# Optimization experiments

Hardware: AMD Instinct MI355X
Metric: run time of the kernel (lower is better)

The kernel has to match this reference:

```python
import jax, jax.numpy as jnp
import numpy as np

NUM_LEVELS = 16
LEVEL_DIM = 2
BASE_RES = 16
DESIRED_RES = 2048
HASHMAP_SIZE = 2 ** 19
MULTIRES = 6
N_POINTS = 1048576

_scale = np.exp2(np.log2(DESIRED_RES / BASE_RES) / (NUM_LEVELS - 1))
RESOLUTIONS = [int(np.ceil(BASE_RES * _scale ** l)) for l in range(NUM_LEVELS)]
PRIMES = np.array([1, 2654435761, 805459861], dtype=np.uint32)
CORNERS = np.array([[i, j, k] for i in (0, 1) for j in (0, 1) for k in (0, 1)], dtype=np.int32)  # [8,3]


def positional_embed(x):
    # NeRF embedding (include_input, log-sampled freqs 2^0..2^(M-1)) -> [N, 3 + 3*2*M] = [N,39]
    freqs = (2.0 ** jnp.arange(MULTIRES)).astype(x.dtype)        # [M]
    xb = x[:, None, :] * freqs[None, :, None]                    # [N, M, 3]
    emb = jnp.concatenate([jnp.sin(xb), jnp.cos(xb)], axis=-1)   # [N, M, 6]
    return jnp.concatenate([x, emb.reshape(x.shape[0], -1)], axis=-1)


def hash_encode(x, tables):
    # multiresolution hash-grid trilinear lookup; x in [0,1]^3 -> [N, NUM_LEVELS*LEVEL_DIM]
    corners = jnp.asarray(CORNERS)       # [8,3]
    primes = jnp.asarray(PRIMES)         # [3] uint32
    outs = []
    for l, R in enumerate(RESOLUTIONS):  # fixed 16 levels (structurally distinct)
        pos = x * (R - 1)                # [N,3]
        p0 = jnp.floor(pos)
        w = pos - p0                     # fractional part, [N,3]
        c = p0.astype(jnp.int32)[:, None, :] + corners[None]   # [N,8,3] corner coords
        c = jnp.clip(c, 0, R - 1)
        if (R ** 3) <= HASHMAP_SIZE:
            idx = c[..., 0] + R * c[..., 1] + R * R * c[..., 2]  # direct (dense) indexing
        else:
            cu = c.astype(jnp.uint32)
            h = (cu[..., 0] * primes[0]) ^ (cu[..., 1] * primes[1]) ^ (cu[..., 2] * primes[2])
            idx = (h & jnp.uint32(HASHMAP_SIZE - 1)).astype(jnp.int32)
        wc = jnp.where(corners[None].astype(bool), w[:, None, :], 1.0 - w[:, None, :])  # [N,8,3]
        wc = jnp.prod(wc, axis=-1)        # trilinear weights [N,8]
        feats = tables[l][idx]            # gather [N,8,LEVEL_DIM]
        outs.append(jnp.sum(wc[..., None] * feats, axis=1))
    return jnp.concatenate(outs, axis=-1)


def softplus100(x):
    # torch.nn.Softplus(beta=100) with default threshold=20 (linear when beta*x > 20)
    return jnp.where(x * 100.0 > 20.0, x, jax.nn.softplus(x * 100.0) / 100.0)


def setup_inputs() -> dict:
    key = jax.random.key(0)
    ks = jax.random.split(key, 8)
    D_IN = 3 + 3 * 2 * MULTIRES + NUM_LEVELS * LEVEL_DIM  # 71
    x = jax.random.uniform(ks[0], (N_POINTS, 3), dtype=jnp.float32)
    tables = jax.random.uniform(ks[1], (NUM_LEVELS, HASHMAP_SIZE, LEVEL_DIM), minval=-1e-4, maxval=1e-4, dtype=jnp.float32)
    W0 = jax.random.normal(ks[2], (64, D_IN), dtype=jnp.float32) * (np.sqrt(2.0) / np.sqrt(64.0))
    b0 = jnp.zeros((64,), jnp.float32)
    W1 = jax.random.normal(ks[3], (64, 64), dtype=jnp.float32) * (np.sqrt(2.0) / np.sqrt(64.0))
    b1 = jnp.zeros((64,), jnp.float32)
    W2 = jnp.full((17, 64), np.sqrt(np.pi) / np.sqrt(64.0), jnp.float32) + jax.random.normal(ks[4], (17, 64), dtype=jnp.float32) * 1e-4
    b2 = jnp.full((17,), -1.0, jnp.float32)  # geometric init bias
    return {"x": x, "tables": tables, "W0": W0, "b0": b0, "W1": W1, "b1": b1, "W2": W2, "b2": b2}


def reference(x, tables, W0, b0, W1, b1, W2, b2):
    # divide_factor = 1.0 -> encoding sees x directly
    feat = hash_encode(x, tables)                                   # [N,32]
    h = jnp.concatenate([positional_embed(x), feat], axis=-1)       # [N,71]
    h = softplus100(h @ W0.T + b0)                                  # [N,64]
    h = softplus100(h @ W1.T + b1)                                  # [N,64]
    return h @ W2.T + b2                                            # [N,17] = (sdf, 16 features)
```

## Files before the change

### kernel.cpp

```cpp
#include <hip/hip_runtime.h>
#include <stdint.h>

#define HMAP   (1u << 19)
#define HMASK  (HMAP - 1u)

typedef short bf16x8 __attribute__((ext_vector_type(8)));
typedef float f32x4  __attribute__((ext_vector_type(4)));
typedef float f32x2  __attribute__((ext_vector_type(2)));
typedef unsigned u32x2 __attribute__((ext_vector_type(2)));

__device__ __constant__ const int c_res[16] = {16, 23, 31, 43, 59, 81, 112, 154, 213, 295, 407, 562, 777, 1073, 1483, 2048};

__device__ __forceinline__ unsigned short f2bf(float f) {
    unsigned u = __float_as_uint(f);
    u += 0x7fffu + ((u >> 16) & 1u);
    return (unsigned short)(u >> 16);
}

__device__ __forceinline__ float softplus100(float v) {
    return fmaxf(v, 0.f) + 0.01f * __logf(1.f + __expf(-100.f * fabsf(v)));
}

__device__ __forceinline__ bf16x8 cvt8(const float* __restrict__ p) {
    f32x4 a = *(const f32x4*)p;
    f32x4 b = *(const f32x4*)(p + 4);
    bf16x8 r;
    r[0] = f2bf(a[0]); r[1] = f2bf(a[1]); r[2] = f2bf(a[2]); r[3] = f2bf(a[3]);
    r[4] = f2bf(b[0]); r[5] = f2bf(b[1]); r[6] = f2bf(b[2]); r[7] = f2bf(b[3]);
    return r;
}

__device__ __forceinline__ float2 upk(unsigned v) {
    return make_float2(__uint_as_float(v << 16), __uint_as_float(v & 0xffff0000u));
}

__device__ __forceinline__ float2 gather_level(const float* __restrict__ tab, int R,
                                               float x0, float x1, float x2) {
    const float Rm1 = (float)(R - 1);
    float px = x0 * Rm1, py = x1 * Rm1, pz = x2 * Rm1;
    float fx = floorf(px), fy = floorf(py), fz = floorf(pz);
    float wx = px - fx, wy = py - fy, wz = pz - fz;
    int ix = (int)fx, iy = (int)fy, iz = (int)fz;
    ix = max(0, min(ix, R - 1)); iy = max(0, min(iy, R - 1)); iz = max(0, min(iz, R - 1));
    int jx = min(ix + 1, R - 1), jy = min(iy + 1, R - 1), jz = min(iz + 1, R - 1);
    float ax = 1.f - wx, ay = 1.f - wy, az = 1.f - wz;
    float wyz0 = ay * az, wyz1 = wy * az, wyz2 = ay * wz, wyz3 = wy * wz;
    float2 lo[4], hi[4];
    const bool adj = (jx == ix + 1);
    if ((long long)R * R * R <= (long long)HMAP) {
        unsigned sy = (unsigned)R, sz = (unsigned)(R * R);
        unsigned bases[4] = {(unsigned)iy * sy + (unsigned)iz * sz,
                             (unsigned)jy * sy + (unsigned)iz * sz,
                             (unsigned)iy * sy + (unsigned)jz * sz,
                             (unsigned)jy * sy + (unsigned)jz * sz};
        const float2* t2 = (const float2*)tab;
        #pragma unroll
        for (int k = 0; k < 4; ++k) {
            unsigned i0 = bases[k] + (unsigned)ix;
            if (adj && !(i0 & 1u)) {
                f32x4 q = *(const f32x4*)(tab + ((size_t)i0 << 1));
                lo[k] = make_float2(q[0], q[1]);
                hi[k] = make_float2(q[2], q[3]);
            } else {
                lo[k] = t2[i0];
                hi[k] = t2[bases[k] + (unsigned)jx];
            }
        }
    } else {
        unsigned hy0 = (unsigned)iy * 2654435761u, hy1 = (unsigned)jy * 2654435761u;
        unsigned hz0 = (unsigned)iz * 805459861u,  hz1 = (unsigned)jz * 805459861u;
        unsigned ms[4] = {hy0 ^ hz0, hy1 ^ hz0, hy0 ^ hz1, hy1 ^ hz1};
        if (adj && ((ix & 1) == 0)) {
            #pragma unroll
            for (int k = 0; k < 4; ++k) {
                unsigned h = ((unsigned)ix ^ ms[k]) & HMASK;
                f32x4 q = *(const f32x4*)(tab + ((size_t)(h & ~1u) << 1));
                float2 e0 = make_float2(q[0], q[1]);
                float2 e1 = make_float2(q[2], q[3]);
                bool sw = (h & 1u) != 0;
                lo[k] = sw ? e1 : e0;
                hi[k] = sw ? e0 : e1;
            }
        } else {
            const float2* t2 = (const float2*)tab;
            #pragma unroll
            for (int k = 0; k < 4; ++k) {
                unsigned hl = ((unsigned)ix ^ ms[k]) & HMASK;
                unsigned hh = ((unsigned)jx ^ ms[k]) & HMASK;
                lo[k] = t2[hl];
                hi[k] = t2[hh];
            }
        }
    }
    float2 r = make_float2(0.f, 0.f);
    float wyz[4] = {wyz0, wyz1, wyz2, wyz3};
    #pragma unroll
    for (int k = 0; k < 4; ++k) {
        float wl = ax * wyz[k], wh = wx * wyz[k];
        r.x += wl * lo[k].x + wh * hi[k].x;
        r.y += wl * lo[k].y + wh * hi[k].y;
    }
    return r;
}

__device__ __forceinline__ void gather2(const float* __restrict__ tab, int R,
                                        float x0A, float x1A, float x2A,
                                        float x0B, float x1B, float x2B,
                                        float2& rA, float2& rB) {
    const float Rm1 = (float)(R - 1);
    float wxv[2], axv[2];
    float wyz[2][4];
    float2 lo[2][4], hi[2][4];
    int ixv[2], jxv[2];
    unsigned basev[2][4];
    const bool dense = (long long)R * R * R <= (long long)HMAP;
    #pragma unroll
    for (int t = 0; t < 2; ++t) {
        const float X0 = t ? x0B : x0A, X1 = t ? x1B : x1A, X2 = t ? x2B : x2A;
        float px = X0 * Rm1, py = X1 * Rm1, pz = X2 * Rm1;
        float fx = floorf(px), fy = floorf(py), fz = floorf(pz);
        float wx = px - fx, wy = py - fy, wz = pz - fz;
        int ix = (int)fx, iy = (int)fy, iz = (int)fz;
        ix = max(0, min(ix, R - 1)); iy = max(0, min(iy, R - 1)); iz = max(0, min(iz, R - 1));
        int jx = min(ix + 1, R - 1), jy = min(iy + 1, R - 1), jz = min(iz + 1, R - 1);
        float ax = 1.f - wx, ay = 1.f - wy, az = 1.f - wz;
        wyz[t][0] = ay * az; wyz[t][1] = wy * az; wyz[t][2] = ay * wz; wyz[t][3] = wy * wz;
        wxv[t] = wx; axv[t] = ax; ixv[t] = ix; jxv[t] = jx;
        if (dense) {
            unsigned sy = (unsigned)R, sz = (unsigned)(R * R);
            basev[t][0] = (unsigned)iy * sy + (unsigned)iz * sz;
            basev[t][1] = (unsigned)jy * sy + (unsigned)iz * sz;
            basev[t][2] = (unsigned)iy * sy + (unsigned)jz * sz;
            basev[t][3] = (unsigned)jy * sy + (unsigned)jz * sz;
        } else {
            unsigned hy0 = (unsigned)iy * 2654435761u, hy1 = (unsigned)jy * 2654435761u;
            unsigned hz0 = (unsigned)iz * 805459861u,  hz1 = (unsigned)jz * 805459861u;
            basev[t][0] = hy0 ^ hz0; basev[t][1] = hy1 ^ hz0;
            basev[t][2] = hy0 ^ hz1; basev[t][3] = hy1 ^ hz1;
        }
    }
    if (dense) {
        const float2* t2 = (const float2*)tab;
        #pragma unroll
        for (int t = 0; t < 2; ++t) {
            const bool adj = (jxv[t] == ixv[t] + 1);
            #pragma unroll
            for (int k = 0; k < 4; ++k) {
                unsigned i0 = basev[t][k] + (unsigned)ixv[t];
                if (adj && !(i0 & 1u)) {
                    f32x4 q = *(const f32x4*)(tab + ((size_t)i0 << 1));
                    lo[t][k] = make_float2(q[0], q[1]);
                    hi[t][k] = make_float2(q[2], q[3]);
                } else {
                    lo[t][k] = t2[i0];
                    hi[t][k] = t2[basev[t][k] + (unsigned)jxv[t]];
                }
            }
        }
    } else {
        const float2* t2 = (const float2*)tab;
        #pragma unroll
        for (int t = 0; t < 2; ++t) {
            const bool adj = (jxv[t] == ixv[t] + 1) && ((ixv[t] & 1) == 0);
            #pragma unroll
            for (int k = 0; k < 4; ++k) {
                if (adj) {
                    unsigned h = ((unsigned)ixv[t] ^ basev[t][k]) & HMASK;
                    f32x4 q = *(const f32x4*)(tab + ((size_t)(h & ~1u) << 1));
                    float2 e0 = make_float2(q[0], q[1]);
                    float2 e1 = make_float2(q[2], q[3]);
                    bool sw = (h & 1u) != 0;
                    lo[t][k] = sw ? e1 : e0;
                    hi[t][k] = sw ? e0 : e1;
                } else {
                    unsigned hl = ((unsigned)ixv[t] ^ basev[t][k]) & HMASK;
                    unsigned hh = ((unsigned)jxv[t] ^ basev[t][k]) & HMASK;
                    lo[t][k] = t2[hl];
                    hi[t][k] = t2[hh];
                }
            }
        }
    }
    float2 res[2];
    #pragma unroll
    for (int t = 0; t < 2; ++t) {
        float2 r = make_float2(0.f, 0.f);
        #pragma unroll
        for (int k = 0; k < 4; ++k) {
            float wl = axv[t] * wyz[t][k], wh = wxv[t] * wyz[t][k];
            r.x += wl * lo[t][k].x + wh * hi[t][k].x;
            r.y += wl * lo[t][k].y + wh * hi[t][k].y;
        }
        res[t] = r;
    }
    rA = res[0]; rB = res[1];
}

__device__ __forceinline__ void gather2h(const unsigned* __restrict__ tab, int R,
                                         float x0A, float x1A, float x2A,
                                         float x0B, float x1B, float x2B,
                                         float2& rA, float2& rB) {
    const float Rm1 = (float)(R - 1);
    float wxv[2], axv[2], wyz[2][4];
    int ixv[2], jxv[2];
    bool adjv[2];
    unsigned msv[2][4];
    #pragma unroll
    for (int t = 0; t < 2; ++t) {
        const float X0 = t ? x0B : x0A, X1 = t ? x1B : x1A, X2 = t ? x2B : x2A;
        float px = X0 * Rm1, py = X1 * Rm1, pz = X2 * Rm1;
        float fx = floorf(px), fy = floorf(py), fz = floorf(pz);
        float wx = px - fx, wy = py - fy, wz = pz - fz;
        int ix = (int)fx, iy = (int)fy, iz = (int)fz;
        ix = max(0, min(ix, R - 1)); iy = max(0, min(iy, R - 1)); iz = max(0, min(iz, R - 1));
        int jx = min(ix + 1, R - 1), jy = min(iy + 1, R - 1), jz = min(iz + 1, R - 1);
        float ax = 1.f - wx, ay = 1.f - wy, az = 1.f - wz;
        wyz[t][0] = ay * az; wyz[t][1] = wy * az; wyz[t][2] = ay * wz; wyz[t][3] = wy * wz;
        wxv[t] = wx; axv[t] = ax; ixv[t] = ix; jxv[t] = jx;
        adjv[t] = (jx == ix + 1) && ((ix & 1) == 0);
        unsigned hy0 = (unsigned)iy * 2654435761u, hy1 = (unsigned)jy * 2654435761u;
        unsigned hz0 = (unsigned)iz * 805459861u,  hz1 = (unsigned)jz * 805459861u;
        msv[t][0] = hy0 ^ hz0; msv[t][1] = hy1 ^ hz0;
        msv[t][2] = hy0 ^ hz1; msv[t][3] = hy1 ^ hz1;
    }
    float2 lo[2][4], hi[2][4];
    #pragma unroll
    for (int t = 0; t < 2; ++t) {
        #pragma unroll
        for (int k = 0; k < 4; ++k) {
            if (adjv[t]) {
                unsigned h = ((unsigned)ixv[t] ^ msv[t][k]) & HMASK;
                u32x2 q = *(const u32x2*)(tab + (h & ~1u));
                float2 e0 = upk(q[0]), e1 = upk(q[1]);
                bool sw = (h & 1u) != 0;
                lo[t][k] = sw ? e1 : e0;
                hi[t][k] = sw ? e0 : e1;
            } else {
                unsigned hl = ((unsigned)ixv[t] ^ msv[t][k]) & HMASK;
                unsigned hh = ((unsigned)jxv[t] ^ msv[t][k]) & HMASK;
                lo[t][k] = upk(tab[hl]);
                hi[t][k] = upk(tab[hh]);
            }
        }
    }
    float2 res[2];
    #pragma unroll
    for (int t = 0; t < 2; ++t) {
        float2 r = make_float2(0.f, 0.f);
        #pragma unroll
        for (int k = 0; k < 4; ++k) {
            float wl = axv[t] * wyz[t][k], wh = wxv[t] * wyz[t][k];
            r.x += wl * lo[t][k].x + wh * hi[t][k].x;
            r.y += wl * lo[t][k].y + wh * hi[t][k].y;
        }
        res[t] = r;
    }
    rA = res[0]; rB = res[1];
}

__global__ __launch_bounds__(256)
void cvt_tables(const float* __restrict__ tables, unsigned* __restrict__ tbf) {
    const size_t i = (size_t)blockIdx.x * 256 + threadIdx.x;
    const f32x2* src = (const f32x2*)(tables + (size_t)5 * 2 * HMAP);
    f32x2 f = __builtin_nontemporal_load(src + i);
    unsigned v = (unsigned)f2bf(f[0]) | ((unsigned)f2bf(f[1]) << 16);
    __builtin_nontemporal_store(v, tbf + i);
}

__global__ __launch_bounds__(256, 6)
void gather_hashed(const float* __restrict__ x, const unsigned* __restrict__ tbf,
                   unsigned* __restrict__ feat, int N) {
    const int j = blockIdx.x & 7;
    const int i = blockIdx.x >> 3;
    int level, chunk;
    if (i < 2048) {
        level = 5 + j; chunk = i;
    } else {
        const int r = i - 2048;
        if (j < 3) {
            const int share = (j == 2) ? 682 : 683;
            if (r >= share) return;
            level = 13; chunk = j * 683 + r;
        } else if (j < 6) {
            const int jj = j - 3;
            const int share = (jj == 2) ? 682 : 683;
            if (r >= share) return;
            level = 14; chunk = jj * 683 + r;
        } else {
            if (r >= 1024) return;
            level = 15; chunk = (j - 6) * 1024 + r;
        }
    }
    const size_t p0 = (size_t)chunk * 512 + 2u * threadIdx.x;
    const f32x2* xv = (const f32x2*)(x + 3 * p0);
    f32x2 u0 = __builtin_nontemporal_load(xv);
    f32x2 u1 = __builtin_nontemporal_load(xv + 1);
    f32x2 u2 = __builtin_nontemporal_load(xv + 2);
    float2 fA, fB;
    gather2h(tbf + (size_t)(level - 5) * HMAP, c_res[level],
             u0[0], u0[1], u1[0],
             u1[1], u2[0], u2[1],
             fA, fB);
    u32x2 v;
    v[0] = (unsigned)f2bf(fA.x) | ((unsigned)f2bf(fA.y) << 16);
    v[1] = (unsigned)f2bf(fB.x) | ((unsigned)f2bf(fB.y) << 16);
    __builtin_nontemporal_store(v, (u32x2*)(feat + (size_t)(level - 5) * N + p0));
}

#define NPB       128
#define TILES     8
#define PTS_BLK   (NPB * TILES)
#define SA_STRIDE 104
#define SW0_OFF   (128 * 104)
#define SMEM_SHORTS (SW0_OFF + 64 * 104)

__global__ __launch_bounds__(256, 4)
void mlp_tiled2(const float* __restrict__ x, const float* __restrict__ tables,
                const unsigned* __restrict__ feat,
                const float* __restrict__ W0, const float* __restrict__ b0,
                const float* __restrict__ W1, const float* __restrict__ b1,
                const float* __restrict__ W2, const float* __restrict__ b2,
                float* __restrict__ out, int N) {
    __shared__ unsigned short smem[SMEM_SHORTS];
    const int tid  = threadIdx.x;
    const int blk  = blockIdx.x;
    const int wave = tid >> 6, lane = tid & 63;
    const int mhalf = (wave & 1) * 64;
    const int nhalf = (wave >> 1);
    const int lrow = lane & 15, quad = lane >> 4;

    for (int i = tid; i < 64 * 104; i += 256) {
        int n = i / 104, k = i - n * 104;
        smem[SW0_OFF + i] = (k < 71) ? f2bf(W0[n * 71 + k]) : (unsigned short)0;
    }
    for (int i = tid; i < 128 * 25; i += 256) {
        int p = i / 25, k = i - p * 25;
        smem[p * SA_STRIDE + 71 + k] = 0;
    }
    bf16x8 w1f[2][2];
    #pragma unroll
    for (int ks = 0; ks < 2; ++ks)
        #pragma unroll
        for (int nt = 0; nt < 2; ++nt) {
            int n = nhalf * 32 + nt * 16 + lrow;
            w1f[ks][nt] = cvt8(W1 + n * 64 + ks * 32 + quad * 8);
        }
    bf16x8 w2f[2];
    {
        int n2 = nhalf * 16 + lrow;
        #pragma unroll
        for (int ks = 0; ks < 2; ++ks) {
            if (n2 < 17) w2f[ks] = cvt8(W2 + n2 * 64 + ks * 32 + quad * 8);
            else { bf16x8 z = {0,0,0,0,0,0,0,0}; w2f[ks] = z; }
        }
    }
    float b0v[2], b1v[2], b2v;
    #pragma unroll
    for (int nt = 0; nt < 2; ++nt) {
        b0v[nt] = b0[nhalf * 32 + nt * 16 + lrow];
        b1v[nt] = b1[nhalf * 32 + nt * 16 + lrow];
    }
    { int c2 = nhalf * 16 + lrow; b2v = (c2 < 17) ? b2[c2] : 0.f; }
    __syncthreads();

    const size_t pbase0 = (size_t)blk * PTS_BLK;
    #pragma unroll 1
    for (int t = 0; t < TILES; ++t) {
        const size_t pb = pbase0 + (size_t)t * NPB;
        {
            const int p = tid & 127;
            const size_t gp = pb + p;
            unsigned short* row = &smem[p * SA_STRIDE];
            const float x0 = __builtin_nontemporal_load(x + 3 * gp);
            const float x1 = __builtin_nontemporal_load(x + 3 * gp + 1);
            const float x2 = __builtin_nontemporal_load(x + 3 * gp + 2);
            float sa, ca, sb, cb, sc, cc;
            __sincosf(x0, &sa, &ca);
            __sincosf(x1, &sb, &cb);
            __sincosf(x2, &sc, &cc);
            if (tid < 128) {
                row[0] = f2bf(x0); row[1] = f2bf(x1); row[2] = f2bf(x2);
                #pragma unroll
                for (int m = 0; m < 6; ++m) {
                    row[3 + 6 * m + 0] = f2bf(sa);
                    row[3 + 6 * m + 1] = f2bf(sb);
                    row[3 + 6 * m + 2] = f2bf(sc);
                    float nsa = 2.f * sa * ca, nca = 1.f - 2.f * sa * sa;
                    float nsb = 2.f * sb * cb, ncb = 1.f - 2.f * sb * sb;
                    float nsc = 2.f * sc * cc, ncc = 1.f - 2.f * sc * sc;
                    sa = nsa; ca = nca; sb = nsb; cb = ncb; sc = nsc; cc = ncc;
                }
                float2 f;
                f = gather_level(tables,                         16, x0, x1, x2);
                row[39] = f2bf(f.x); row[40] = f2bf(f.y);
                f = gather_level(tables + (size_t)1 * 2 * HMAP,  23, x0, x1, x2);
                row[41] = f2bf(f.x); row[42] = f2bf(f.y);
                f = gather_level(tables + (size_t)2 * 2 * HMAP,  31, x0, x1, x2);
                row[43] = f2bf(f.x); row[44] = f2bf(f.y);
            } else {
                #pragma unroll
                for (int m = 0; m < 6; ++m) {
                    row[3 + 6 * m + 3] = f2bf(ca);
                    row[3 + 6 * m + 4] = f2bf(cb);
                    row[3 + 6 * m + 5] = f2bf(cc);
                    float nsa = 2.f * sa * ca, nca = 1.f - 2.f * sa * sa;
                    float nsb = 2.f * sb * cb, ncb = 1.f - 2.f * sb * sb;
                    float nsc = 2.f * sc * cc, ncc = 1.f - 2.f * sc * sc;
                    sa = nsa; ca = nca; sb = nsb; cb = ncb; sc = nsc; cc = ncc;
                }
                float2 f;
                f = gather_level(tables + (size_t)3 * 2 * HMAP,  43, x0, x1, x2);
                row[45] = f2bf(f.x); row[46] = f2bf(f.y);
                f = gather_level(tables + (size_t)4 * 2 * HMAP,  59, x0, x1, x2);
                row[47] = f2bf(f.x); row[48] = f2bf(f.y);
                #pragma unroll
                for (int li = 0; li < 11; ++li) {
                    unsigned v = __builtin_nontemporal_load(feat + (size_t)li * N + gp);
                    row[49 + 2 * li] = (unsigned short)(v & 0xffffu);
                    row[50 + 2 * li] = (unsigned short)(v >> 16);
                }
            }
        }
        __syncthreads();

        f32x4 acc0[4][2];
        #pragma unroll
        for (int mt = 0; mt < 4; ++mt)
            #pragma unroll
            for (int nt = 0; nt < 2; ++nt) acc0[mt][nt] = (f32x4){0.f, 0.f, 0.f, 0.f};
        #pragma unroll
        for (int ks = 0; ks < 3; ++ks) {
            bf16x8 bfr[2];
            #pragma unroll
            for (int nt = 0; nt < 2; ++nt) {
                int n = nhalf * 32 + nt * 16 + lrow;
                bfr[nt] = *(const bf16x8*)&smem[SW0_OFF + n * 104 + ks * 32 + quad * 8];
            }
            #pragma unroll
            for (int mt = 0; mt < 4; ++mt) {
                int m = mhalf + mt * 16 + lrow;
                bf16x8 afr = *(const bf16x8*)&smem[m * SA_STRIDE + ks * 32 + quad * 8];
                #pragma unroll
                for (int nt = 0; nt < 2; ++nt)
                    acc0[mt][nt] = __builtin_amdgcn_mfma_f32_16x16x32_bf16(afr, bfr[nt], acc0[mt][nt], 0, 0, 0);
            }
        }
        __syncthreads();
        #pragma unroll
        for (int mt = 0; mt < 4; ++mt)
            #pragma unroll
            for (int nt = 0; nt < 2; ++nt) {
                int colg = nhalf * 32 + nt * 16 + lrow;
                #pragma unroll
                for (int r = 0; r < 4; ++r) {
                    int rowm = mhalf + mt * 16 + quad * 4 + r;
                    smem[rowm * SA_STRIDE + colg] = f2bf(softplus100(acc0[mt][nt][r] + b0v[nt]));
                }
            }
        __syncthreads();

        f32x4 acc1[4][2];
        #pragma unroll
        for (int mt = 0; mt < 4; ++mt)
            #pragma unroll
            for (int nt = 0; nt < 2; ++nt) acc1[mt][nt] = (f32x4){0.f, 0.f, 0.f, 0.f};
        #pragma unroll
        for (int ks = 0; ks < 2; ++ks) {
            #pragma unroll
            for (int mt = 0; mt < 4; ++mt) {
                int m = mhalf + mt * 16 + lrow;
                bf16x8 afr = *(const bf16x8*)&smem[m * SA_STRIDE + ks * 32 + quad * 8];
                #pragma unroll
                for (int nt = 0; nt < 2; ++nt)
                    acc1[mt][nt] = __builtin_amdgcn_mfma_f32_16x16x32_bf16(afr, w1f[ks][nt], acc1[mt][nt], 0, 0, 0);
            }
        }
        __syncthreads();
        #pragma unroll
        for (int mt = 0; mt < 4; ++mt)
            #pragma unroll
            for (int nt = 0; nt < 2; ++nt) {
                int colg = nhalf * 32 + nt * 16 + lrow;
                #pragma unroll
                for (int r = 0; r < 4; ++r) {
                    int rowm = mhalf + mt * 16 + quad * 4 + r;
                    smem[rowm * SA_STRIDE + colg] = f2bf(softplus100(acc1[mt][nt][r] + b1v[nt]));
                }
            }
        __syncthreads();

        f32x4 acc2[4];
        #pragma unroll
        for (int mt = 0; mt < 4; ++mt) acc2[mt] = (f32x4){0.f, 0.f, 0.f, 0.f};
        #pragma unroll
        for (int ks = 0; ks < 2; ++ks) {
            #pragma unroll
            for (int mt = 0; mt < 4; ++mt) {
                int m = mhalf + mt * 16 + lrow;
                bf16x8 afr = *(const bf16x8*)&smem[m * SA_STRIDE + ks * 32 + quad * 8];
                acc2[mt] = __builtin_amdgcn_mfma_f32_16x16x32_bf16(afr, w2f[ks], acc2[mt], 0, 0, 0);
            }
        }
        {
            int colg = nhalf * 16 + lrow;
            if (colg < 17) {
                #pragma unroll
                for (int mt = 0; mt < 4; ++mt)
                    #pragma unroll
                    for (int r = 0; r < 4; ++r) {
                        int rowm = mhalf + mt * 16 + quad * 4 + r;
                        __builtin_nontemporal_store(acc2[mt][r] + b2v,
                                                    out + (pb + rowm) * 17 + colg);
                    }
            }
        }
        __syncthreads();
    }
}

__global__ __launch_bounds__(256, 6)
void gather_levels(const float* __restrict__ x, const float* __restrict__ tables,
                   unsigned* __restrict__ feat, int N, int C) {
    const int b = blockIdx.x;
    const int half = 8 * C;
    int r, level;
    if (b < half) { r = b; level = r & 7; }
    else          { r = b - half; level = 15 - (r & 7); }
    const size_t p0 = (size_t)(r >> 3) * 512 + 2u * threadIdx.x;
    const f32x2* xv = (const f32x2*)(x + 3 * p0);
    f32x2 u0 = __builtin_nontemporal_load(xv);
    f32x2 u1 = __builtin_nontemporal_load(xv + 1);
    f32x2 u2 = __builtin_nontemporal_load(xv + 2);
    float2 fA, fB;
    gather2(tables + (size_t)level * (2u * HMAP), c_res[level],
            u0[0], u0[1], u1[0],
            u1[1], u2[0], u2[1],
            fA, fB);
    u32x2 v;
    v[0] = (unsigned)f2bf(fA.x) | ((unsigned)f2bf(fA.y) << 16);
    v[1] = (unsigned)f2bf(fB.x) | ((unsigned)f2bf(fB.y) << 16);
    __builtin_nontemporal_store(v, (u32x2*)(feat + (size_t)level * N + p0));
}

__global__ __launch_bounds__(256, 4)
void mlp_tiled(const float* __restrict__ x, const unsigned* __restrict__ feat,
               const float* __restrict__ W0, const float* __restrict__ b0,
               const float* __restrict__ W1, const float* __restrict__ b1,
               const float* __restrict__ W2, const float* __restrict__ b2,
               float* __restrict__ out, int N) {
    __shared__ unsigned short smem[SMEM_SHORTS];
    const int tid  = threadIdx.x;
    const int blk  = blockIdx.x;
    const int wave = tid >> 6, lane = tid & 63;
    const int mhalf = (wave & 1) * 64;
    const int nhalf = (wave >> 1);
    const int lrow = lane & 15, quad = lane >> 4;

    for (int i = tid; i < 64 * 104; i += 256) {
        int n = i / 104, k = i - n * 104;
        smem[SW0_OFF + i] = (k < 71) ? f2bf(W0[n * 71 + k]) : (unsigned short)0;
    }
    for (int i = tid; i < 128 * 25; i += 256) {
        int p = i / 25, k = i - p * 25;
        smem[p * SA_STRIDE + 71 + k] = 0;
    }
    bf16x8 w1f[2][2];
    #pragma unroll
    for (int ks = 0; ks < 2; ++ks)
        #pragma unroll
        for (int nt = 0; nt < 2; ++nt) {
            int n = nhalf * 32 + nt * 16 + lrow;
            w1f[ks][nt] = cvt8(W1 + n * 64 + ks * 32 + quad * 8);
        }
    bf16x8 w2f[2];
    {
        int n2 = nhalf * 16 + lrow;
        #pragma unroll
        for (int ks = 0; ks < 2; ++ks) {
            if (n2 < 17) w2f[ks] = cvt8(W2 + n2 * 64 + ks * 32 + quad * 8);
            else { bf16x8 z = {0,0,0,0,0,0,0,0}; w2f[ks] = z; }
        }
    }
    float b0v[2], b1v[2], b2v;
    #pragma unroll
    for (int nt = 0; nt < 2; ++nt) {
        b0v[nt] = b0[nhalf * 32 + nt * 16 + lrow];
        b1v[nt] = b1[nhalf * 32 + nt * 16 + lrow];
    }
    { int c2 = nhalf * 16 + lrow; b2v = (c2 < 17) ? b2[c2] : 0.f; }
    __syncthreads();

    const size_t pbase0 = (size_t)blk * PTS_BLK;
    #pragma unroll 1
    for (int t = 0; t < TILES; ++t) {
        const size_t pb = pbase0 + (size_t)t * NPB;
        {
            const int p = tid & 127;
            const size_t gp = pb + p;
            unsigned short* row = &smem[p * SA_STRIDE];
            const float x0 = __builtin_nontemporal_load(x + 3 * gp);
            const float x1 = __builtin_nontemporal_load(x + 3 * gp + 1);
            const float x2 = __builtin_nontemporal_load(x + 3 * gp + 2);
            if (tid < 128) {
                row[0] = f2bf(x0); row[1] = f2bf(x1); row[2] = f2bf(x2);
                float fr = 1.f;
                #pragma unroll
                for (int m = 0; m < 6; ++m) {
                    row[3 + 6 * m + 0] = f2bf(__sinf(x0 * fr));
                    row[3 + 6 * m + 1] = f2bf(__sinf(x1 * fr));
                    row[3 + 6 * m + 2] = f2bf(__sinf(x2 * fr));
                    fr *= 2.f;
                }
            } else {
                float fr = 1.f;
                #pragma unroll
                for (int m = 0; m < 6; ++m) {
                    row[3 + 6 * m + 3] = f2bf(__cosf(x0 * fr));
                    row[3 + 6 * m + 4] = f2bf(__cosf(x1 * fr));
                    row[3 + 6 * m + 5] = f2bf(__cosf(x2 * fr));
                    fr *= 2.f;
                }
                #pragma unroll
                for (int l = 0; l < 16; ++l) {
                    unsigned v = __builtin_nontemporal_load(feat + (size_t)l * N + gp);
                    row[39 + 2 * l] = (unsigned short)(v & 0xffffu);
                    row[40 + 2 * l] = (unsigned short)(v >> 16);
                }
            }
        }
        __syncthreads();

        f32x4 acc0[4][2];
        #pragma unroll
        for (int mt = 0; mt < 4; ++mt)
            #pragma unroll
            for (int nt = 0; nt < 2; ++nt) acc0[mt][nt] = (f32x4){0.f, 0.f, 0.f, 0.f};
        #pragma unroll
        for (int ks = 0; ks < 3; ++ks) {
            bf16x8 bfr[2];
            #pragma unroll
            for (int nt = 0; nt < 2; ++nt) {
                int n = nhalf * 32 + nt * 16 + lrow;
                bfr[nt] = *(const bf16x8*)&smem[SW0_OFF + n * 104 + ks * 32 + quad * 8];
            }
            #pragma unroll
            for (int mt = 0; mt < 4; ++mt) {
                int m = mhalf + mt * 16 + lrow;
                bf16x8 afr = *(const bf16x8*)&smem[m * SA_STRIDE + ks * 32 + quad * 8];
                #pragma unroll
                for (int nt = 0; nt < 2; ++nt)
                    acc0[mt][nt] = __builtin_amdgcn_mfma_f32_16x16x32_bf16(afr, bfr[nt], acc0[mt][nt], 0, 0, 0);
            }
        }
        __syncthreads();
        #pragma unroll
        for (int mt = 0; mt < 4; ++mt)
            #pragma unroll
            for (int nt = 0; nt < 2; ++nt) {
                int colg = nhalf * 32 + nt * 16 + lrow;
                #pragma unroll
                for (int r = 0; r < 4; ++r) {
                    int rowm = mhalf + mt * 16 + quad * 4 + r;
                    smem[rowm * SA_STRIDE + colg] = f2bf(softplus100(acc0[mt][nt][r] + b0v[nt]));
                }
            }
        __syncthreads();

        f32x4 acc1[4][2];
        #pragma unroll
        for (int mt = 0; mt < 4; ++mt)
            #pragma unroll
            for (int nt = 0; nt < 2; ++nt) acc1[mt][nt] = (f32x4){0.f, 0.f, 0.f, 0.f};
        #pragma unroll
        for (int ks = 0; ks < 2; ++ks) {
            #pragma unroll
            for (int mt = 0; mt < 4; ++mt) {
                int m = mhalf + mt * 16 + lrow;
                bf16x8 afr = *(const bf16x8*)&smem[m * SA_STRIDE + ks * 32 + quad * 8];
                #pragma unroll
                for (int nt = 0; nt < 2; ++nt)
                    acc1[mt][nt] = __builtin_amdgcn_mfma_f32_16x16x32_bf16(afr, w1f[ks][nt], acc1[mt][nt], 0, 0, 0);
            }
        }
        __syncthreads();
        #pragma unroll
        for (int mt = 0; mt < 4; ++mt)
            #pragma unroll
            for (int nt = 0; nt < 2; ++nt) {
                int colg = nhalf * 32 + nt * 16 + lrow;
                #pragma unroll
                for (int r = 0; r < 4; ++r) {
                    int rowm = mhalf + mt * 16 + quad * 4 + r;
                    smem[rowm * SA_STRIDE + colg] = f2bf(softplus100(acc1[mt][nt][r] + b1v[nt]));
                }
            }
        __syncthreads();

        f32x4 acc2[4];
        #pragma unroll
        for (int mt = 0; mt < 4; ++mt) acc2[mt] = (f32x4){0.f, 0.f, 0.f, 0.f};
        #pragma unroll
        for (int ks = 0; ks < 2; ++ks) {
            #pragma unroll
            for (int mt = 0; mt < 4; ++mt) {
                int m = mhalf + mt * 16 + lrow;
                bf16x8 afr = *(const bf16x8*)&smem[m * SA_STRIDE + ks * 32 + quad * 8];
                acc2[mt] = __builtin_amdgcn_mfma_f32_16x16x32_bf16(afr, w2f[ks], acc2[mt], 0, 0, 0);
            }
        }
        {
            int colg = nhalf * 16 + lrow;
            if (colg < 17) {
                #pragma unroll
                for (int mt = 0; mt < 4; ++mt)
                    #pragma unroll
                    for (int r = 0; r < 4; ++r) {
                        int rowm = mhalf + mt * 16 + quad * 4 + r;
                        __builtin_nontemporal_store(acc2[mt][r] + b2v,
                                                    out + (pb + rowm) * 17 + colg);
                    }
            }
        }
        __syncthreads();
    }
}

__global__ __launch_bounds__(256, 3)
void gn_fused(const float* __restrict__ x, const float* __restrict__ tables,
              const float* __restrict__ W0, const float* __restrict__ b0,
              const float* __restrict__ W1, const float* __restrict__ b1,
              const float* __restrict__ W2, const float* __restrict__ b2,
              float* __restrict__ out) {
    __shared__ unsigned short smem[SMEM_SHORTS];
    const int tid = threadIdx.x;
    const int blk = blockIdx.x;
    const int wave = tid >> 6, lane = tid & 63;
    const int mhalf = (wave & 1) * 64;
    const int nhalf = (wave >> 1);
    const int lrow = lane & 15, quad = lane >> 4;
    for (int i = tid; i < 64 * 104; i += 256) {
        int n = i / 104, k = i - n * 104;
        smem[SW0_OFF + i] = (k < 71) ? f2bf(W0[n * 71 + k]) : (unsigned short)0;
    }
    for (int i = tid; i < 128 * 25; i += 256) {
        int p = i / 25, k = i - p * 25;
        smem[p * SA_STRIDE + 71 + k] = 0;
    }
    bf16x8 w1f[2][2];
    #pragma unroll
    for (int ks = 0; ks < 2; ++ks)
        #pragma unroll
        for (int nt = 0; nt < 2; ++nt) {
            int n = nhalf * 32 + nt * 16 + lrow;
            w1f[ks][nt] = cvt8(W1 + n * 64 + ks * 32 + quad * 8);
        }
    bf16x8 w2f[2];
    {
        int n2 = nhalf * 16 + lrow;
        #pragma unroll
        for (int ks = 0; ks < 2; ++ks) {
            if (n2 < 17) w2f[ks] = cvt8(W2 + n2 * 64 + ks * 32 + quad * 8);
            else { bf16x8 z = {0,0,0,0,0,0,0,0}; w2f[ks] = z; }
        }
    }
    float b0v[2], b1v[2], b2v;
    #pragma unroll
    for (int nt = 0; nt < 2; ++nt) {
        b0v[nt] = b0[nhalf * 32 + nt * 16 + lrow];
        b1v[nt] = b1[nhalf * 32 + nt * 16 + lrow];
    }
    { int c2 = nhalf * 16 + lrow; b2v = (c2 < 17) ? b2[c2] : 0.f; }
    {
        const int p = tid & 127;
        const size_t gp = (size_t)blk * NPB + p;
        const float x0 = x[3 * gp], x1 = x[3 * gp + 1], x2 = x[3 * gp + 2];
        unsigned short* row = &smem[p * SA_STRIDE];
        if (tid < 128) {
            row[0] = f2bf(x0); row[1] = f2bf(x1); row[2] = f2bf(x2);
            float fr = 1.f;
            #pragma unroll
            for (int m = 0; m < 6; ++m) {
                row[3 + 6 * m + 0] = f2bf(__sinf(x0 * fr));
                row[3 + 6 * m + 1] = f2bf(__sinf(x1 * fr));
                row[3 + 6 * m + 2] = f2bf(__sinf(x2 * fr));
                fr *= 2.f;
            }
            #pragma unroll
            for (int li = 0; li < 8; ++li) {
                const int l = 2 * li;
                float2 f = gather_level(tables + (size_t)l * (2u * HMAP), c_res[l], x0, x1, x2);
                row[39 + 2 * l] = f2bf(f.x);
                row[40 + 2 * l] = f2bf(f.y);
            }
        } else {
            float fr = 1.f;
            #pragma unroll
            for (int m = 0; m < 6; ++m) {
                row[3 + 6 * m + 3] = f2bf(__cosf(x0 * fr));
                row[3 + 6 * m + 4] = f2bf(__cosf(x1 * fr));
                row[3 + 6 * m + 5] = f2bf(__cosf(x2 * fr));
                fr *= 2.f;
            }
            #pragma unroll
            for (int li = 0; li < 8; ++li) {
                const int l = 2 * li + 1;
                float2 f = gather_level(tables + (size_t)l * (2u * HMAP), c_res[l], x0, x1, x2);
                row[39 + 2 * l] = f2bf(f.x);
                row[40 + 2 * l] = f2bf(f.y);
            }
        }
    }
    __syncthreads();
    f32x4 acc0[4][2];
    #pragma unroll
    for (int mt = 0; mt < 4; ++mt)
        #pragma unroll
        for (int nt = 0; nt < 2; ++nt) acc0[mt][nt] = (f32x4){0.f, 0.f, 0.f, 0.f};
    #pragma unroll
    for (int ks = 0; ks < 3; ++ks) {
        bf16x8 bfr[2];
        #pragma unroll
        for (int nt = 0; nt < 2; ++nt) {
            int n = nhalf * 32 + nt * 16 + lrow;
            bfr[nt] = *(const bf16x8*)&smem[SW0_OFF + n * 104 + ks * 32 + quad * 8];
        }
        #pragma unroll
        for (int mt = 0; mt < 4; ++mt) {
            int m = mhalf + mt * 16 + lrow;
            bf16x8 afr = *(const bf16x8*)&smem[m * SA_STRIDE + ks * 32 + quad * 8];
            #pragma unroll
            for (int nt = 0; nt < 2; ++nt)
                acc0[mt][nt] = __builtin_amdgcn_mfma_f32_16x16x32_bf16(afr, bfr[nt], acc0[mt][nt], 0, 0, 0);
        }
    }
    __syncthreads();
    #pragma unroll
    for (int mt = 0; mt < 4; ++mt)
        #pragma unroll
        for (int nt = 0; nt < 2; ++nt) {
            int colg = nhalf * 32 + nt * 16 + lrow;
            #pragma unroll
            for (int r = 0; r < 4; ++r) {
                int rowm = mhalf + mt * 16 + quad * 4 + r;
                smem[rowm * SA_STRIDE + colg] = f2bf(softplus100(acc0[mt][nt][r] + b0v[nt]));
            }
        }
    __syncthreads();
    f32x4 acc1[4][2];
    #pragma unroll
    for (int mt = 0; mt < 4; ++mt)
        #pragma unroll
        for (int nt = 0; nt < 2; ++nt) acc1[mt][nt] = (f32x4){0.f, 0.f, 0.f, 0.f};
    #pragma unroll
    for (int ks = 0; ks < 2; ++ks) {
        #pragma unroll
        for (int mt = 0; mt < 4; ++mt) {
            int m = mhalf + mt * 16 + lrow;
            bf16x8 afr = *(const bf16x8*)&smem[m * SA_STRIDE + ks * 32 + quad * 8];
            #pragma unroll
            for (int nt = 0; nt < 2; ++nt)
                acc1[mt][nt] = __builtin_amdgcn_mfma_f32_16x16x32_bf16(afr, w1f[ks][nt], acc1[mt][nt], 0, 0, 0);
        }
    }
    __syncthreads();
    #pragma unroll
    for (int mt = 0; mt < 4; ++mt)
        #pragma unroll
        for (int nt = 0; nt < 2; ++nt) {
            int colg = nhalf * 32 + nt * 16 + lrow;
            #pragma unroll
            for (int r = 0; r < 4; ++r) {
                int rowm = mhalf + mt * 16 + quad * 4 + r;
                smem[rowm * SA_STRIDE + colg] = f2bf(softplus100(acc1[mt][nt][r] + b1v[nt]));
            }
        }
    __syncthreads();
    f32x4 acc2[4];
    #pragma unroll
    for (int mt = 0; mt < 4; ++mt) acc2[mt] = (f32x4){0.f, 0.f, 0.f, 0.f};
    #pragma unroll
    for (int ks = 0; ks < 2; ++ks) {
        #pragma unroll
        for (int mt = 0; mt < 4; ++mt) {
            int m = mhalf + mt * 16 + lrow;
            bf16x8 afr = *(const bf16x8*)&smem[m * SA_STRIDE + ks * 32 + quad * 8];
            acc2[mt] = __builtin_amdgcn_mfma_f32_16x16x32_bf16(afr, w2f[ks], acc2[mt], 0, 0, 0);
        }
    }
    {
        int colg = nhalf * 16 + lrow;
        if (colg < 17) {
            #pragma unroll
            for (int mt = 0; mt < 4; ++mt)
                #pragma unroll
                for (int r = 0; r < 4; ++r) {
                    int rowm = mhalf + mt * 16 + quad * 4 + r;
                    out[((size_t)blk * NPB + rowm) * 17 + colg] = acc2[mt][r] + b2v;
                }
        }
    }
}

extern "C" void kernel_launch(void* const* d_in, const int* in_sizes, int n_in,
                              void* d_out, int out_size, void* d_ws, size_t ws_size,
                              hipStream_t stream) {
    const float* x      = (const float*)d_in[0];
    const float* tables = (const float*)d_in[1];
    const float* W0     = (const float*)d_in[2];
    const float* b0     = (const float*)d_in[3];
    const float* W1     = (const float*)d_in[4];
    const float* b1     = (const float*)d_in[5];
    const float* W2     = (const float*)d_in[6];
    const float* b2     = (const float*)d_in[7];
    float* out = (float*)d_out;
    const int n = in_sizes[0] / 3;
    const size_t featA_b = (size_t)11 * n * 4;
    const size_t tbf_b   = (size_t)11 * HMAP * 4;
    const size_t wsB     = (size_t)16 * n * 4;
    if (n == (1 << 20) && ws_size >= featA_b + tbf_b) {
        unsigned* feat = (unsigned*)d_ws;
        unsigned* tbf  = (unsigned*)((char*)d_ws + featA_b);
        cvt_tables<<<dim3(11 * HMAP / 256), dim3(256), 0, stream>>>(tables, tbf);
        gather_hashed<<<dim3(8 * 3072), dim3(256), 0, stream>>>(x, tbf, feat, n);
        mlp_tiled2<<<dim3(n / PTS_BLK), dim3(256), 0, stream>>>(x, tables, feat, W0, b0, W1, b1, W2, b2, out, n);
    } else if (ws_size >= wsB) {
        unsigned* feat = (unsigned*)d_ws;
        const int C = n / 512;
        gather_levels<<<dim3(16 * C), dim3(256), 0, stream>>>(x, tables, feat, n, C);
        mlp_tiled<<<dim3(n / PTS_BLK), dim3(256), 0, stream>>>(x, feat, W0, b0, W1, b1, W2, b2, out, n);
    } else {
        gn_fused<<<dim3(n / NPB), dim3(256), 0, stream>>>(x, tables, W0, b0, W1, b1, W2, b2, out);
    }
}
```

Baseline: 549.4 us.

## Pipeline hashed gather and MLP across point chunks in a fused kernel

Replaces the separate hashed-gather kernel and MLP kernel with a single fused_step kernel launched nine times over 131072-point chunks. Each launch gathers hashed features for chunk s while running the MLP on chunk s-1, so memory-bound gathers and MFMA compute can overlap within one grid. The cost is more launches, per-launch weight reloads into LDS with fewer tiles per MLP block, and possible tail imbalance between the two block roles.

```diff
diff --git a/kernel.cpp b/kernel.cpp
--- a/kernel.cpp
+++ b/kernel.cpp
@@ -267,74 +267,82 @@
     __builtin_nontemporal_store(v, tbf + i);
 }
 
-__global__ __launch_bounds__(256, 6)
-void gather_hashed(const float* __restrict__ x, const unsigned* __restrict__ tbf,
-                   unsigned* __restrict__ feat, int N) {
-    const int j = blockIdx.x & 7;
-    const int i = blockIdx.x >> 3;
-    int level, chunk;
-    if (i < 2048) {
-        level = 5 + j; chunk = i;
-    } else {
-        const int r = i - 2048;
-        if (j < 3) {
-            const int share = (j == 2) ? 682 : 683;
-            if (r >= share) return;
-            level = 13; chunk = j * 683 + r;
-        } else if (j < 6) {
-            const int jj = j - 3;
-            const int share = (jj == 2) ? 682 : 683;
-            if (r >= share) return;
-            level = 14; chunk = jj * 683 + r;
-        } else {
-            if (r >= 1024) return;
-            level = 15; chunk = (j - 6) * 1024 + r;
-        }
-    }
-    const size_t p0 = (size_t)chunk * 512 + 2u * threadIdx.x;
-    const f32x2* xv = (const f32x2*)(x + 3 * p0);
-    f32x2 u0 = __builtin_nontemporal_load(xv);
-    f32x2 u1 = __builtin_nontemporal_load(xv + 1);
-    f32x2 u2 = __builtin_nontemporal_load(xv + 2);
-    float2 fA, fB;
-    gather2h(tbf + (size_t)(level - 5) * HMAP, c_res[level],
-             u0[0], u0[1], u1[0],
-             u1[1], u2[0], u2[1],
-             fA, fB);
-    u32x2 v;
-    v[0] = (unsigned)f2bf(fA.x) | ((unsigned)f2bf(fA.y) << 16);
-    v[1] = (unsigned)f2bf(fB.x) | ((unsigned)f2bf(fB.y) << 16);
-    __builtin_nontemporal_store(v, (u32x2*)(feat + (size_t)(level - 5) * N + p0));
-}
-
 #define NPB       128
-#define TILES     8
-#define PTS_BLK   (NPB * TILES)
 #define SA_STRIDE 104
 #define SW0_OFF   (128 * 104)
 #define SMEM_SHORTS (SW0_OFF + 64 * 104)
 
+#define CHUNK     131072
+#define MLP_SLOTS 32
+#define GSLOTS    384
+#define FSTEP_GRID (8 * (MLP_SLOTS + GSLOTS))
+#define TILES_F   4
+
 __global__ __launch_bounds__(256, 4)
-void mlp_tiled2(const float* __restrict__ x, const float* __restrict__ tables,
-                const unsigned* __restrict__ feat,
+void fused_step(const float* __restrict__ x, const float* __restrict__ tables,
+                const unsigned* __restrict__ tbf, unsigned* __restrict__ feat,
                 const float* __restrict__ W0, const float* __restrict__ b0,
                 const float* __restrict__ W1, const float* __restrict__ b1,
                 const float* __restrict__ W2, const float* __restrict__ b2,
-                float* __restrict__ out, int N) {
+                float* __restrict__ out, int N, int cg, int cm) {
     __shared__ unsigned short smem[SMEM_SHORTS];
+    const int j = blockIdx.x & 7;
+    const int i = blockIdx.x >> 3;
+
+    if (i >= MLP_SLOTS) {
+        if (cg < 0) return;
+        const int g = i - MLP_SLOTS;
+        int level, row;
+        if (g < 256) { level = 5 + j; row = g; }
+        else {
+            const int r = g - 256;
+            if (j < 3) {
+                const int base = (j == 0) ? 0 : (j == 1 ? 86 : 171);
+                const int share = (j == 0) ? 86 : 85;
+                if (r >= share) return;
+                level = 13; row = base + r;
+            } else if (j < 6) {
+                const int jj = j - 3;
+                const int base = (jj == 0) ? 0 : (jj == 1 ? 86 : 171);
+                const int share = (jj == 0) ? 86 : 85;
+                if (r >= share) return;
+                level = 14; row = base + r;
+            } else {
+                if (r >= 128) return;
+                level = 15; row = (j - 6) * 128 + r;
+            }
+        }
+        const size_t p0 = (size_t)cg * CHUNK + (size_t)row * 512 + 2u * threadIdx.x;
+        const f32x2* xv = (const f32x2*)(x + 3 * p0);
+        f32x2 u0 = __builtin_nontemporal_load(xv);
+        f32x2 u1 = __builtin_nontemporal_load(xv + 1);
+        f32x2 u2 = __builtin_nontemporal_load(xv + 2);
+        float2 fA, fB;
+        gather2h(tbf + (size_t)(level - 5) * HMAP, c_res[level],
+                 u0[0], u0[1], u1[0],
+                 u1[1], u2[0], u2[1],
+                 fA, fB);
+        u32x2 v;
+        v[0] = (unsigned)f2bf(fA.x) | ((unsigned)f2bf(fA.y) << 16);
+        v[1] = (unsigned)f2bf(fB.x) | ((unsigned)f2bf(fB.y) << 16);
+        __builtin_nontemporal_store(v, (u32x2*)(feat + (size_t)(level - 5) * N + p0));
+        return;
+    }
+
+    if (cm < 0) return;
+    const int m = i * 8 + j;
     const int tid  = threadIdx.x;
-    const int blk  = blockIdx.x;
     const int wave = tid >> 6, lane = tid & 63;
     const int mhalf = (wave & 1) * 64;
     const int nhalf = (wave >> 1);
     const int lrow = lane & 15, quad = lane >> 4;
 
-    for (int i = tid; i < 64 * 104; i += 256) {
-        int n = i / 104, k = i - n * 104;
-        smem[SW0_OFF + i] = (k < 71) ? f2bf(W0[n * 71 + k]) : (unsigned short)0;
-    }
-    for (int i = tid; i < 128 * 25; i += 256) {
-        int p = i / 25, k = i - p * 25;
+    for (int q = tid; q < 64 * 104; q += 256) {
+        int n = q / 104, k = q - n * 104;
+        smem[SW0_OFF + q] = (k < 71) ? f2bf(W0[n * 71 + k]) : (unsigned short)0;
+    }
+    for (int q = tid; q < 128 * 25; q += 256) {
+        int p = q / 25, k = q - p * 25;
         smem[p * SA_STRIDE + 71 + k] = 0;
     }
     bf16x8 w1f[2][2];
@@ -363,9 +371,9 @@
     { int c2 = nhalf * 16 + lrow; b2v = (c2 < 17) ? b2[c2] : 0.f; }
     __syncthreads();
 
-    const size_t pbase0 = (size_t)blk * PTS_BLK;
+    const size_t pbase0 = (size_t)cm * CHUNK + (size_t)m * (NPB * TILES_F);
     #pragma unroll 1
-    for (int t = 0; t < TILES; ++t) {
+    for (int t = 0; t < TILES_F; ++t) {
         const size_t pb = pbase0 + (size_t)t * NPB;
         {
             const int p = tid & 127;
@@ -381,10 +389,10 @@
             if (tid < 128) {
                 row[0] = f2bf(x0); row[1] = f2bf(x1); row[2] = f2bf(x2);
                 #pragma unroll
-                for (int m = 0; m < 6; ++m) {
-                    row[3 + 6 * m + 0] = f2bf(sa);
-                    row[3 + 6 * m + 1] = f2bf(sb);
-                    row[3 + 6 * m + 2] = f2bf(sc);
+                for (int mm = 0; mm < 6; ++mm) {
+                    row[3 + 6 * mm + 0] = f2bf(sa);
+                    row[3 + 6 * mm + 1] = f2bf(sb);
+                    row[3 + 6 * mm + 2] = f2bf(sc);
                     float nsa = 2.f * sa * ca, nca = 1.f - 2.f * sa * sa;
                     float nsb = 2.f * sb * cb, ncb = 1.f - 2.f * sb * sb;
                     float nsc = 2.f * sc * cc, ncc = 1.f - 2.f * sc * sc;
@@ -399,10 +407,10 @@
                 row[43] = f2bf(f.x); row[44] = f2bf(f.y);
             } else {
                 #pragma unroll
-                for (int m = 0; m < 6; ++m) {
-                    row[3 + 6 * m + 3] = f2bf(ca);
-                    row[3 + 6 * m + 4] = f2bf(cb);
-                    row[3 + 6 * m + 5] = f2bf(cc);
+                for (int mm = 0; mm < 6; ++mm) {
+                    row[3 + 6 * mm + 3] = f2bf(ca);
+                    row[3 + 6 * mm + 4] = f2bf(cb);
+                    row[3 + 6 * mm + 5] = f2bf(cc);
                     float nsa = 2.f * sa * ca, nca = 1.f - 2.f * sa * sa;
                     float nsb = 2.f * sb * cb, ncb = 1.f - 2.f * sb * sb;
                     float nsc = 2.f * sc * cc, ncc = 1.f - 2.f * sc * sc;
@@ -438,8 +446,8 @@
             }
             #pragma unroll
             for (int mt = 0; mt < 4; ++mt) {
-                int m = mhalf + mt * 16 + lrow;
-                bf16x8 afr = *(const bf16x8*)&smem[m * SA_STRIDE + ks * 32 + quad * 8];
+                int mr = mhalf + mt * 16 + lrow;
+                bf16x8 afr = *(const bf16x8*)&smem[mr * SA_STRIDE + ks * 32 + quad * 8];
                 #pragma unroll
                 for (int nt = 0; nt < 2; ++nt)
                     acc0[mt][nt] = __builtin_amdgcn_mfma_f32_16x16x32_bf16(afr, bfr[nt], acc0[mt][nt], 0, 0, 0);
@@ -468,8 +476,8 @@
         for (int ks = 0; ks < 2; ++ks) {
             #pragma unroll
             for (int mt = 0; mt < 4; ++mt) {
-                int m = mhalf + mt * 16 + lrow;
-                bf16x8 afr = *(const bf16x8*)&smem[m * SA_STRIDE + ks * 32 + quad * 8];
+                int mr = mhalf + mt * 16 + lrow;
+                bf16x8 afr = *(const bf16x8*)&smem[mr * SA_STRIDE + ks * 32 + quad * 8];
                 #pragma unroll
                 for (int nt = 0; nt < 2; ++nt)
                     acc1[mt][nt] = __builtin_amdgcn_mfma_f32_16x16x32_bf16(afr, w1f[ks][nt], acc1[mt][nt], 0, 0, 0);
@@ -496,8 +504,8 @@
         for (int ks = 0; ks < 2; ++ks) {
             #pragma unroll
             for (int mt = 0; mt < 4; ++mt) {
-                int m = mhalf + mt * 16 + lrow;
-                bf16x8 afr = *(const bf16x8*)&smem[m * SA_STRIDE + ks * 32 + quad * 8];
+                int mr = mhalf + mt * 16 + lrow;
+                bf16x8 afr = *(const bf16x8*)&smem[mr * SA_STRIDE + ks * 32 + quad * 8];
                 acc2[mt] = __builtin_amdgcn_mfma_f32_16x16x32_bf16(afr, w2f[ks], acc2[mt], 0, 0, 0);
             }
         }
@@ -517,6 +525,9 @@
         __syncthreads();
     }
 }
+
+#define TILES     8
+#define PTS_BLK   (NPB * TILES)
 
 __global__ __launch_bounds__(256, 6)
 void gather_levels(const float* __restrict__ x, const float* __restrict__ tables,
@@ -921,8 +932,12 @@
         unsigned* feat = (unsigned*)d_ws;
         unsigned* tbf  = (unsigned*)((char*)d_ws + featA_b);
         cvt_tables<<<dim3(11 * HMAP / 256), dim3(256), 0, stream>>>(tables, tbf);
-        gather_hashed<<<dim3(8 * 3072), dim3(256), 0, stream>>>(x, tbf, feat, n);
-        mlp_tiled2<<<dim3(n / PTS_BLK), dim3(256), 0, stream>>>(x, tables, feat, W0, b0, W1, b1, W2, b2, out, n);
+        for (int s = 0; s <= 8; ++s) {
+            const int cg = (s < 8) ? s : -1;
+            const int cm = s - 1;
+            fused_step<<<dim3(FSTEP_GRID), dim3(256), 0, stream>>>(
+                x, tables, tbf, feat, W0, b0, W1, b1, W2, b2, out, n, cg, cm);
+        }
     } else if (ws_size >= wsB) {
         unsigned* feat = (unsigned*)d_ws;
         const int C = n / 512;
```

Result: slower. 720.8 us (+31.2%).

## Pack dense levels into bf16 2x2 quad layout for vectorized gathers

Applied to the files above, without the earlier changes.

Adds a preprocessing kernel that converts the five dense low-resolution levels into bf16 2x2 xy-quads stored as 16-byte vectors. The MLP kernel then fetches each z-slice's four corners with one to four 128-bit loads instead of eight scattered float2 loads from the fp32 tables. It also raises gather_hashed's occupancy hint from 6 to 8 waves. The cost is an extra small kernel launch, more workspace, and bf16 rounding of the dense-level table values.

```diff
diff --git a/kernel.cpp b/kernel.cpp
--- a/kernel.cpp
+++ b/kernel.cpp
@@ -8,6 +8,7 @@
 typedef float f32x4  __attribute__((ext_vector_type(4)));
 typedef float f32x2  __attribute__((ext_vector_type(2)));
 typedef unsigned u32x2 __attribute__((ext_vector_type(2)));
+typedef unsigned u32x4 __attribute__((ext_vector_type(4)));
 
 __device__ __constant__ const int c_res[16] = {16, 23, 31, 43, 59, 81, 112, 154, 213, 295, 407, 562, 777, 1073, 1483, 2048};
 
@@ -32,6 +33,10 @@
 
 __device__ __forceinline__ float2 upk(unsigned v) {
     return make_float2(__uint_as_float(v << 16), __uint_as_float(v & 0xffff0000u));
+}
+
+__device__ __forceinline__ unsigned pkf2(float2 f) {
+    return (unsigned)f2bf(f.x) | ((unsigned)f2bf(f.y) << 16);
 }
 
 __device__ __forceinline__ float2 gather_level(const float* __restrict__ tab, int R,
@@ -102,6 +107,49 @@
     }
     return r;
 }
+
+__device__ __forceinline__ unsigned qel(u32x4 q, int sx, int sy) {
+    unsigned a = sx ? q[1] : q[0];
+    unsigned b = sx ? q[3] : q[2];
+    return sy ? b : a;
+}
+
+__device__ __forceinline__ float2 gather_q(const unsigned* __restrict__ qt, int R, int nxq,
+                                           float X0, float X1, float X2) {
+    const float Rm1 = (float)(R - 1);
+    float px = X0 * Rm1, py = X1 * Rm1, pz = X2 * Rm1;
+    float fx = floorf(px), fy = floorf(py), fz = floorf(pz);
+    float wx = px - fx, wy = py - fy, wz = pz - fz;
+    int ix = (int)fx, iy = (int)fy, iz = (int)fz;
+    ix = max(0, min(ix, R - 1)); iy = max(0, min(iy, R - 1)); iz = max(0, min(iz, R - 1));
+    int jx = min(ix + 1, R - 1), jy = min(iy + 1, R - 1), jz = min(iz + 1, R - 1);
+    float ax = 1.f - wx, ay = 1.f - wy, az = 1.f - wz;
+    const int qx0 = ix >> 1, qy0 = iy >> 1;
+    const bool hx = (jx >> 1) != qx0, hy = (jy >> 1) != qy0;
+    const int sxi = ix & 1, syi = iy & 1, sxj = jx & 1, syj = jy & 1;
+    const float w00 = ax * ay, w10 = wx * ay, w01 = ax * wy, w11 = wx * wy;
+    const int zz[2] = {iz, jz};
+    float2 pv[2];
+    #pragma unroll
+    for (int p = 0; p < 2; ++p) {
+        const unsigned* base = qt + ((size_t)(zz[p] * nxq + qy0) * nxq + qx0) * 4;
+        u32x4 q00 = *(const u32x4*)base;
+        u32x4 q10 = q00, q01 = q00, q11;
+        if (hx) q10 = *(const u32x4*)(base + 4);
+        if (hy) q01 = *(const u32x4*)(base + 4 * nxq);
+        if (hx && hy) q11 = *(const u32x4*)(base + 4 * nxq + 4);
+        else          q11 = hx ? q10 : q01;
+        float2 v00 = upk(qel(q00, sxi, syi));
+        float2 v10 = upk(qel(q10, sxj, syi));
+        float2 v01 = upk(qel(q01, sxi, syj));
+        float2 v11 = upk(qel(q11, sxj, syj));
+        pv[p].x = w00 * v00.x + w10 * v10.x + w01 * v01.x + w11 * v11.x;
+        pv[p].y = w00 * v00.y + w10 * v10.y + w01 * v01.y + w11 * v11.y;
+    }
+    return make_float2(az * pv[0].x + wz * pv[1].x, az * pv[0].y + wz * pv[1].y);
+}
+
+#define QD_TOTAL 86184
 
 __device__ __forceinline__ void gather2(const float* __restrict__ tab, int R,
                                         float x0A, float x1A, float x2A,
@@ -267,7 +315,32 @@
     __builtin_nontemporal_store(v, tbf + i);
 }
 
-__global__ __launch_bounds__(256, 6)
+__global__ __launch_bounds__(256)
+void cvt_dense(const float* __restrict__ tables, unsigned* __restrict__ qd) {
+    const int i = blockIdx.x * 256 + threadIdx.x;
+    if (i >= QD_TOTAL) return;
+    int l, R, nx, base;
+    if      (i < 1024)  { l = 0; R = 16; nx = 8;  base = 0; }
+    else if (i < 4336)  { l = 1; R = 23; nx = 12; base = 1024; }
+    else if (i < 12272) { l = 2; R = 31; nx = 16; base = 4336; }
+    else if (i < 33084) { l = 3; R = 43; nx = 22; base = 12272; }
+    else                { l = 4; R = 59; nx = 30; base = 33084; }
+    int lq = i - base;
+    int qx = lq % nx; int t = lq / nx; int qy = t % nx; int z = t / nx;
+    int x0 = 2 * qx, x1 = min(x0 + 1, R - 1);
+    int y0 = 2 * qy, y1 = min(y0 + 1, R - 1);
+    const float2* src = (const float2*)(tables + (size_t)l * 2 * HMAP);
+    const int zb = R * R * z;
+    float2 a = src[x0 + R * y0 + zb];
+    float2 b = src[x1 + R * y0 + zb];
+    float2 c = src[x0 + R * y1 + zb];
+    float2 d = src[x1 + R * y1 + zb];
+    u32x4 v;
+    v[0] = pkf2(a); v[1] = pkf2(b); v[2] = pkf2(c); v[3] = pkf2(d);
+    *(u32x4*)(qd + 4 * (size_t)i) = v;
+}
+
+__global__ __launch_bounds__(256, 8)
 void gather_hashed(const float* __restrict__ x, const unsigned* __restrict__ tbf,
                    unsigned* __restrict__ feat, int N) {
     const int j = blockIdx.x & 7;
@@ -316,7 +389,7 @@
 
 __global__ __launch_bounds__(256, 4)
 void mlp_tiled2(const float* __restrict__ x, const float* __restrict__ tables,
-                const unsigned* __restrict__ feat,
+                const unsigned* __restrict__ qd, const unsigned* __restrict__ feat,
                 const float* __restrict__ W0, const float* __restrict__ b0,
                 const float* __restrict__ W1, const float* __restrict__ b1,
                 const float* __restrict__ W2, const float* __restrict__ b2,
@@ -391,12 +464,21 @@
                     sa = nsa; ca = nca; sb = nsb; cb = ncb; sc = nsc; cc = ncc;
                 }
                 float2 f;
-                f = gather_level(tables,                         16, x0, x1, x2);
-                row[39] = f2bf(f.x); row[40] = f2bf(f.y);
-                f = gather_level(tables + (size_t)1 * 2 * HMAP,  23, x0, x1, x2);
-                row[41] = f2bf(f.x); row[42] = f2bf(f.y);
-                f = gather_level(tables + (size_t)2 * 2 * HMAP,  31, x0, x1, x2);
-                row[43] = f2bf(f.x); row[44] = f2bf(f.y);
+                if (qd) {
+                    f = gather_q(qd,              16,  8, x0, x1, x2);
+                    row[39] = f2bf(f.x); row[40] = f2bf(f.y);
+                    f = gather_q(qd + 4 * 1024,   23, 12, x0, x1, x2);
+                    row[41] = f2bf(f.x); row[42] = f2bf(f.y);
+                    f = gather_q(qd + 4 * 4336,   31, 16, x0, x1, x2);
+                    row[43] = f2bf(f.x); row[44] = f2bf(f.y);
+                } else {
+                    f = gather_level(tables,                        16, x0, x1, x2);
+                    row[39] = f2bf(f.x); row[40] = f2bf(f.y);
+                    f = gather_level(tables + (size_t)1 * 2 * HMAP, 23, x0, x1, x2);
+                    row[41] = f2bf(f.x); row[42] = f2bf(f.y);
+                    f = gather_level(tables + (size_t)2 * 2 * HMAP, 31, x0, x1, x2);
+                    row[43] = f2bf(f.x); row[44] = f2bf(f.y);
+                }
             } else {
                 #pragma unroll
                 for (int m = 0; m < 6; ++m) {
@@ -409,10 +491,17 @@
                     sa = nsa; ca = nca; sb = nsb; cb = ncb; sc = nsc; cc = ncc;
                 }
                 float2 f;
-                f = gather_level(tables + (size_t)3 * 2 * HMAP,  43, x0, x1, x2);
-                row[45] = f2bf(f.x); row[46] = f2bf(f.y);
-                f = gather_level(tables + (size_t)4 * 2 * HMAP,  59, x0, x1, x2);
-                row[47] = f2bf(f.x); row[48] = f2bf(f.y);
+                if (qd) {
+                    f = gather_q(qd + 4 * 12272,  43, 22, x0, x1, x2);
+                    row[45] = f2bf(f.x); row[46] = f2bf(f.y);
+                    f = gather_q(qd + 4 * 33084,  59, 30, x0, x1, x2);
+                    row[47] = f2bf(f.x); row[48] = f2bf(f.y);
+                } else {
+                    f = gather_level(tables + (size_t)3 * 2 * HMAP, 43, x0, x1, x2);
+                    row[45] = f2bf(f.x); row[46] = f2bf(f.y);
+                    f = gather_level(tables + (size_t)4 * 2 * HMAP, 59, x0, x1, x2);
+                    row[47] = f2bf(f.x); row[48] = f2bf(f.y);
+                }
                 #pragma unroll
                 for (int li = 0; li < 11; ++li) {
                     unsigned v = __builtin_nontemporal_load(feat + (size_t)li * N + gp);
@@ -916,13 +1005,22 @@
     const int n = in_sizes[0] / 3;
     const size_t featA_b = (size_t)11 * n * 4;
     const size_t tbf_b   = (size_t)11 * HMAP * 4;
+    const size_t qd_b    = (size_t)QD_TOTAL * 16;
     const size_t wsB     = (size_t)16 * n * 4;
-    if (n == (1 << 20) && ws_size >= featA_b + tbf_b) {
+    if (n == (1 << 20) && ws_size >= featA_b + tbf_b + qd_b) {
+        unsigned* feat = (unsigned*)d_ws;
+        unsigned* tbf  = (unsigned*)((char*)d_ws + featA_b);
+        unsigned* qd   = (unsigned*)((char*)d_ws + featA_b + tbf_b);
+        cvt_tables<<<dim3(11 * HMAP / 256), dim3(256), 0, stream>>>(tables, tbf);
+        cvt_dense<<<dim3((QD_TOTAL + 255) / 256), dim3(256), 0, stream>>>(tables, qd);
+        gather_hashed<<<dim3(8 * 3072), dim3(256), 0, stream>>>(x, tbf, feat, n);
+        mlp_tiled2<<<dim3(n / PTS_BLK), dim3(256), 0, stream>>>(x, tables, qd, feat, W0, b0, W1, b1, W2, b2, out, n);
+    } else if (n == (1 << 20) && ws_size >= featA_b + tbf_b) {
         unsigned* feat = (unsigned*)d_ws;
         unsigned* tbf  = (unsigned*)((char*)d_ws + featA_b);
         cvt_tables<<<dim3(11 * HMAP / 256), dim3(256), 0, stream>>>(tables, tbf);
         gather_hashed<<<dim3(8 * 3072), dim3(256), 0, stream>>>(x, tbf, feat, n);
-        mlp_tiled2<<<dim3(n / PTS_BLK), dim3(256), 0, stream>>>(x, tables, feat, W0, b0, W1, b1, W2, b2, out, n);
+        mlp_tiled2<<<dim3(n / PTS_BLK), dim3(256), 0, stream>>>(x, tables, (const unsigned*)nullptr, feat, W0, b0, W1, b1, W2, b2, out, n);
     } else if (ws_size >= wsB) {
         unsigned* feat = (unsigned*)d_ws;
         const int C = n / 512;
```

Result: no change. 554.8 us (+1.0%).
